# Kernel optimization log

Hardware: AMD Instinct MI355X
Metric: run time of the kernel (lower is better)

Reference implementation:

```python
import jax, jax.numpy as jnp
import numpy as np
import math

B, T, DIM = 2, 2048, 4096
N_HEADS, N_KV_HEADS = 32, 8
HEAD_DIM = DIM // N_HEADS          # 128
N_REP = N_HEADS // N_KV_HEADS      # 4
ROPE_THETA = 500000.0
NEG_INF = -1e9


def setup_inputs() -> dict:
    key = jax.random.key(0)
    ks = jax.random.split(key, 5)
    x = jax.random.normal(ks[0], (B, T, DIM), dtype=jnp.float32)
    # rotary angles: theta_j = pos * base^(-2j/d), shape [T, HEAD_DIM//2]
    inv_freq = 1.0 / (ROPE_THETA ** (jnp.arange(0, HEAD_DIM, 2, dtype=jnp.float32) / HEAD_DIM))
    freqs = jnp.arange(T, dtype=jnp.float32)[:, None] * inv_freq[None, :]
    # causal additive mask [T, T]
    mask = jnp.where(jnp.tril(jnp.ones((T, T), dtype=bool)), 0.0, NEG_INF).astype(jnp.float32)
    s = 0.02
    wq = jax.random.normal(ks[1], (DIM, N_HEADS * HEAD_DIM), dtype=jnp.float32) * s
    wk = jax.random.normal(ks[2], (DIM, N_KV_HEADS * HEAD_DIM), dtype=jnp.float32) * s
    wv = jax.random.normal(ks[3], (DIM, N_KV_HEADS * HEAD_DIM), dtype=jnp.float32) * s
    wo = jax.random.normal(ks[4], (N_HEADS * HEAD_DIM, DIM), dtype=jnp.float32) * s
    return {"x": x, "freqs": freqs, "mask": mask, "wq": wq, "wk": wk, "wv": wv, "wo": wo, "start_pos": 0}


def _apply_rope(x, cos, sin):
    # x: [B, T, H, D]; cos/sin: [T, D//2]; adjacent pairs rotated (view-as-complex)
    xr = x[..., 0::2]
    xi = x[..., 1::2]
    c = cos[None, :, None, :]
    s = sin[None, :, None, :]
    out_r = xr * c - xi * s
    out_i = xr * s + xi * c
    return jnp.stack([out_r, out_i], axis=-1).reshape(x.shape)


def reference(x, freqs, mask, wq, wk, wv, wo, start_pos):
    Bx, Tx, C = x.shape
    xq = (x @ wq).reshape(Bx, Tx, N_HEADS, HEAD_DIM)
    xk = (x @ wk).reshape(Bx, Tx, N_KV_HEADS, HEAD_DIM)
    xv = (x @ wv).reshape(Bx, Tx, N_KV_HEADS, HEAD_DIM)
    cos, sin = jnp.cos(freqs), jnp.sin(freqs)
    xq = _apply_rope(xq, cos, sin)
    xk = _apply_rope(xk, cos, sin)
    # repeat_kv for GQA: [B, T, Hkv, D] -> [B, T, Hkv*n_rep, D]
    xk = jnp.repeat(xk, N_REP, axis=2)
    xv = jnp.repeat(xv, N_REP, axis=2)
    q = xq.transpose(0, 2, 1, 3)  # [B, H, T, D]
    k = xk.transpose(0, 2, 1, 3)
    v = xv.transpose(0, 2, 1, 3)
    scores = jnp.einsum("bhtd,bhsd->bhts", q, k) / math.sqrt(HEAD_DIM)
    scores = scores + mask[None, None, :, :]
    probs = jax.nn.softmax(scores.astype(jnp.float32), axis=-1).astype(q.dtype)
    out = jnp.einsum("bhts,bhsd->bhtd", probs, v)
    out = out.transpose(0, 2, 1, 3).reshape(Bx, Tx, -1)
    return out @ wo
```

## Files before the change

kernel.cpp:

```cpp
#include <hip/hip_runtime.h>
#include <cstdint>
#include <cstddef>

typedef float  f32x4  __attribute__((ext_vector_type(4)));
typedef short  bf16x8 __attribute__((ext_vector_type(8)));
typedef unsigned short u16;
typedef u16    u16x8  __attribute__((ext_vector_type(8)));

#define T_SEQ 2048
#define N_HEADS 32
#define N_KVH 8
#define HD 128

__device__ __forceinline__ u16 f2bf(float f){
  union { float f; unsigned u; } v; v.f = f;
  unsigned u = v.u;
  u += 0x7fffu + ((u >> 16) & 1u);
  return (u16)(u >> 16);
}

__device__ __forceinline__ void gll16(const void* g, void* l){
  __builtin_amdgcn_global_load_lds((const __attribute__((address_space(1))) void*)g,
                                   (__attribute__((address_space(3))) void*)l, 16, 0, 0);
}

__global__ void mk_tables(const float* __restrict__ f, float* __restrict__ c, float* __restrict__ s){
  int i = blockIdx.x*256 + threadIdx.x;
  float v = f[i];
  c[i] = cosf(v);
  s[i] = sinf(v);
}

__global__ void cvt_bf16(const float* __restrict__ in, u16* __restrict__ out){
  size_t i = (size_t)blockIdx.x*256 + threadIdx.x;
  const float4* p = (const float4*)(in + i*8);
  float4 a = p[0], b = p[1];
  u16x8 o;
  o[0]=f2bf(a.x); o[1]=f2bf(a.y); o[2]=f2bf(a.z); o[3]=f2bf(a.w);
  o[4]=f2bf(b.x); o[5]=f2bf(b.y); o[6]=f2bf(b.z); o[7]=f2bf(b.w);
  *(u16x8*)(out + i*8) = o;
}

__global__ void wtrans(const float* __restrict__ W, u16* __restrict__ Wt, int K, int N){
  __shared__ float t[32][33];
  int tx = threadIdx.x, ty = threadIdx.y;
  int nb = blockIdx.x*32, kb = blockIdx.y*32;
#pragma unroll
  for (int j=0;j<4;j++) t[ty+8*j][tx] = W[(size_t)(kb+ty+8*j)*N + nb + tx];
  __syncthreads();
#pragma unroll
  for (int j=0;j<4;j++) Wt[(size_t)(nb+ty+8*j)*K + kb + tx] = f2bf(t[tx][ty+8*j]);
}

__global__ __launch_bounds__(256) void gemm_bf16(
    const u16* __restrict__ A, const u16* __restrict__ Bt,
    float* __restrict__ C, int N, int K)
{
  __shared__ u16 Al[4096];
  __shared__ u16 Bl[4096];
  const int tid = threadIdx.x;
  const int wid = tid >> 6, lane = tid & 63;
  const int lo = lane & 15, hi = lane >> 4;
  const int m0 = blockIdx.y << 7, n0 = blockIdx.x << 7;
  const int wm = (wid >> 1)*64, wn = (wid & 1)*64;

  f32x4 acc[4][4];
#pragma unroll
  for (int i=0;i<4;i++)
#pragma unroll
    for (int j=0;j<4;j++) acc[i][j] = (f32x4){0.f,0.f,0.f,0.f};

  const int r0 = wid*32 + (lane >> 2);
  const int cb = (lane & 3)*8;
  const u16* Ag0 = A  + (size_t)(m0 + r0)*K + cb;
  const u16* Ag1 = Ag0 + (size_t)16*K;
  const u16* Bg0 = Bt + (size_t)(n0 + r0)*K + cb;
  const u16* Bg1 = Bg0 + (size_t)16*K;
  u16* Al0 = &Al[wid*1024]; u16* Al1 = Al0 + 512;
  u16* Bl0 = &Bl[wid*1024]; u16* Bl1 = Bl0 + 512;

  for (int kt = 0; kt < K; kt += 32){
    __syncthreads();
    gll16(Ag0 + kt, Al0);
    gll16(Ag1 + kt, Al1);
    gll16(Bg0 + kt, Bl0);
    gll16(Bg1 + kt, Bl1);
    __syncthreads();
    bf16x8 a[4], b[4];
#pragma unroll
    for (int i=0;i<4;i++){
      a[i] = *(const bf16x8*)&Al[(wm + i*16 + lo)*32 + hi*8];
      b[i] = *(const bf16x8*)&Bl[(wn + i*16 + lo)*32 + hi*8];
    }
#pragma unroll
    for (int i=0;i<4;i++)
#pragma unroll
      for (int j=0;j<4;j++)
        acc[i][j] = __builtin_amdgcn_mfma_f32_16x16x32_bf16(a[i], b[j], acc[i][j], 0, 0, 0);
  }

  float* Cb = C + (size_t)(m0 + wm + hi*4)*N + n0 + wn + lo;
#pragma unroll
  for (int i=0;i<4;i++)
#pragma unroll
    for (int j=0;j<4;j++)
#pragma unroll
      for (int r=0;r<4;r++)
        Cb[(size_t)(i*16 + r)*N + j*16] = acc[i][j][r];
}

__global__ __launch_bounds__(512, 2) void gemm256(
    const u16* __restrict__ A, const u16* __restrict__ Bt,
    float* __restrict__ C, int N, int K)
{
  __shared__ u16 Ab[2][16384];
  __shared__ u16 Bb[2][16384];
  const int tid = threadIdx.x;
  const int w = tid >> 6, lane = tid & 63;
  const int lo = lane & 15, hi = lane >> 4;

  const int nbx = N >> 8;
  const int cpx = (int)gridDim.x >> 3;
  const int swzb = ((int)blockIdx.x & 7)*cpx + ((int)blockIdx.x >> 3);
  const int bx = swzb % nbx, by = swzb / nbx;
  const int m0 = by << 8, n0 = bx << 8;
  const int wm = w >> 2, wn = w & 3;

  const int rA = tid >> 3;
  const int chg = (tid & 7) ^ (rA & 7);
  const size_t srcoff = (size_t)rA * K + chg*8;
  const u16* Ag = A  + (size_t)m0*K + srcoff;
  const u16* Bg = Bt + (size_t)n0*K + srcoff;
  const int dstc = (w*64)*8;

  f32x4 acc[8][4];
#pragma unroll
  for (int i=0;i<8;i++)
#pragma unroll
    for (int j=0;j<4;j++) acc[i][j] = (f32x4){0.f,0.f,0.f,0.f};

  const int NT = K >> 6;
#pragma unroll
  for (int j=0;j<4;j++) gll16(Ag + (size_t)j*64*K, &Ab[0][j*4096 + dstc]);
#pragma unroll
  for (int j=0;j<4;j++) gll16(Bg + (size_t)j*64*K, &Bb[0][j*4096 + dstc]);

  const int sw = lo & 7;
#pragma unroll 1
  for (int t=0; t<NT; ++t){
    const int cur = t & 1;
    if (t > 0){
      asm volatile("s_waitcnt lgkmcnt(0)" ::: "memory");
      __builtin_amdgcn_s_barrier();
    }
    if (t + 1 < NT){
      const int kt = (t+1) << 6;
      const int nxt = cur ^ 1;
#pragma unroll
      for (int j=0;j<4;j++) gll16(Ag + (size_t)j*64*K + kt, &Ab[nxt][j*4096 + dstc]);
#pragma unroll
      for (int j=0;j<4;j++) gll16(Bg + (size_t)j*64*K + kt, &Bb[nxt][j*4096 + dstc]);
      asm volatile("s_waitcnt vmcnt(8)" ::: "memory");
    } else {
      asm volatile("s_waitcnt vmcnt(0)" ::: "memory");
    }
    __builtin_amdgcn_s_barrier();
    __builtin_amdgcn_sched_barrier(0);

    const u16* Ac = &Ab[cur][0] + (wm*128)*64;
    const u16* Bc = &Bb[cur][0] + (wn*64)*64;
    bf16x8 a[4], b[4];
#pragma unroll
    for (int ks=0; ks<2; ks++){
      const int ch = ((ks*4 + hi) ^ sw) << 3;
#pragma unroll
      for (int g=0; g<4; g++) b[g] = *(const bf16x8*)(Bc + (g*16 + lo)*64 + ch);
#pragma unroll
      for (int mh=0; mh<2; mh++){
#pragma unroll
        for (int f=0; f<4; f++) a[f] = *(const bf16x8*)(Ac + (mh*64 + f*16 + lo)*64 + ch);
        __builtin_amdgcn_s_setprio(1);
#pragma unroll
        for (int f=0; f<4; f++)
#pragma unroll
          for (int g=0; g<4; g++)
            acc[mh*4+f][g] = __builtin_amdgcn_mfma_f32_16x16x32_bf16(a[f], b[g], acc[mh*4+f][g], 0, 0, 0);
        __builtin_amdgcn_s_setprio(0);
      }
    }
  }

#pragma unroll
  for (int mh=0; mh<2; mh++)
#pragma unroll
    for (int f=0; f<4; f++)
#pragma unroll
      for (int g=0; g<4; g++)
#pragma unroll
        for (int r=0; r<4; r++)
          C[(size_t)(m0 + wm*128 + mh*64 + f*16 + hi*4 + r)*N + n0 + wn*64 + g*16 + lo] = acc[mh*4+f][g][r];
}

__global__ void rope_q(const float* __restrict__ qf, const float* __restrict__ c,
                       const float* __restrict__ s, u16* __restrict__ qb){
  const int row = blockIdx.x;
  const int t = row & (T_SEQ-1);
  const float* ib = qf + (size_t)row*4096;
  u16* ob = qb + (size_t)row*4096;
#pragma unroll
  for (int k=0;k<8;k++){
    int p = threadIdx.x + k*256;
    int i = p & 63;
    float cv = c[t*64+i], sv = s[t*64+i];
    float2 v = *(const float2*)(ib + 2*p);
    float vr = v.x*cv - v.y*sv;
    float vi = v.x*sv + v.y*cv;
    ushort2 o; o.x = f2bf(vr*0.12751743648963412f); o.y = f2bf(vi*0.12751743648963412f);
    *(ushort2*)(ob + 2*p) = o;
  }
}

__global__ void rope_k(const float* __restrict__ kvf, const float* __restrict__ c,
                       const float* __restrict__ s, u16* __restrict__ kb){
  const int row = blockIdx.x;
  const int b = row >> 11, t = row & (T_SEQ-1);
  const float* ib = kvf + (size_t)row*2048;
#pragma unroll
  for (int k=0;k<2;k++){
    int p = threadIdx.x + k*256;
    int kvh = p >> 6, i = p & 63;
    float cv = c[t*64+i], sv = s[t*64+i];
    float2 v = *(const float2*)(ib + 2*p);
    float vr = v.x*cv - v.y*sv;
    float vi = v.x*sv + v.y*cv;
    u16* o = kb + ((size_t)(b*N_KVH+kvh)*T_SEQ + t)*HD + 2*i;
    ushort2 ov; ov.x = f2bf(vr); ov.y = f2bf(vi);
    *(ushort2*)o = ov;
  }
}

__global__ void vtrans(const float* __restrict__ kvf, u16* __restrict__ vt){
  __shared__ float tl[32][33];
  int tx = threadIdx.x, ty = threadIdx.y;
  int t0 = blockIdx.x*32, d0 = blockIdx.y*32, bh = blockIdx.z;
  int b = bh >> 3, kvh = bh & 7;
#pragma unroll
  for (int j=0;j<4;j++)
    tl[ty+8*j][tx] = kvf[(size_t)(b*T_SEQ + t0+ty+8*j)*2048 + 1024 + kvh*HD + d0 + tx];
  __syncthreads();
#pragma unroll
  for (int j=0;j<4;j++)
    vt[((size_t)bh*HD + d0+ty+8*j)*T_SEQ + t0 + tx] = f2bf(tl[tx][ty+8*j]);
}

#define KVB 64
__global__ __launch_bounds__(512, 2) void attn_kernel(
    const u16* __restrict__ qb, const u16* __restrict__ kb,
    const u16* __restrict__ vt, u16* __restrict__ attn)
{
  __shared__ u16 KV[2][2][8192];
  __shared__ u16 Pl[8][2048];

  const int tid = threadIdx.x;
  const int lane = tid & 63, wid = tid >> 6;
  const int lo = lane & 15, hi = lane >> 4;
  const int pairI = blockIdx.x;
  const int h = blockIdx.y, b = blockIdx.z;
  const int kvh = h >> 2;

  int koff[2], voff[2];
#pragma unroll
  for (int p=0;p<2;p++){
    int s = p*512 + tid;
    int kr = s >> 4, kch = (s & 15) ^ (kr & 7);
    koff[p] = kr*HD + kch*8;
    int vd = s >> 3, vch = (s & 7) ^ (vd & 7);
    voff[p] = vd*T_SEQ + vch*8;
  }
  const u16* Kg = kb + (size_t)(b*N_KVH + kvh)*T_SEQ*HD;
  const u16* Vg = vt + (size_t)(b*N_KVH + kvh)*HD*T_SEQ;

#pragma unroll 1
  for (int pass=0; pass<2; ++pass){
    const int qt = pass ? pairI : (7 - pairI);
    const int q0 = qt*256 + wid*32;
    const int ntiles = (qt+1)*4;

    bf16x8 qfr[2][4];
#pragma unroll
    for (int mb=0;mb<2;mb++){
      const u16* qrow = qb + (size_t)(b*T_SEQ + q0 + mb*16 + lo)*4096 + h*HD;
#pragma unroll
      for (int kc=0;kc<4;kc++) qfr[mb][kc] = *(const bf16x8*)(qrow + kc*32 + hi*8);
    }

    f32x4 acc[2][8];
#pragma unroll
    for (int mb=0;mb<2;mb++)
#pragma unroll
      for (int nd=0;nd<8;nd++) acc[mb][nd] = (f32x4){0.f,0.f,0.f,0.f};
    float m_[2][4], l_[2][4];
#pragma unroll
    for (int mb=0;mb<2;mb++)
#pragma unroll
      for (int r=0;r<4;r++){ m_[mb][r] = -3.0e38f; l_[mb][r] = 0.f; }

    if (pass){
      asm volatile("s_waitcnt lgkmcnt(0)" ::: "memory");
      __builtin_amdgcn_s_barrier();
    }
#pragma unroll
    for (int p=0;p<2;p++){
      gll16(Kg + koff[p], (u16*)&KV[0][0][0] + (p*512 + wid*64)*8);
      gll16(Vg + voff[p], (u16*)&KV[0][1][0] + (p*512 + wid*64)*8);
    }

#pragma unroll 1
    for (int st=0; st<ntiles; ++st){
      const int cur = st & 1;
      const int sb = st*KVB;
      if (st > 0){
        asm volatile("s_waitcnt lgkmcnt(0)" ::: "memory");
        __builtin_amdgcn_s_barrier();
      }
      if (st + 1 < ntiles){
        const int nxt = cur ^ 1;
        const int nb2 = (st+1)*KVB;
#pragma unroll
        for (int p=0;p<2;p++){
          gll16(Kg + nb2*HD + koff[p], (u16*)&KV[nxt][0][0] + (p*512 + wid*64)*8);
          gll16(Vg + nb2    + voff[p], (u16*)&KV[nxt][1][0] + (p*512 + wid*64)*8);
        }
        asm volatile("s_waitcnt vmcnt(4)" ::: "memory");
      } else {
        asm volatile("s_waitcnt vmcnt(0)" ::: "memory");
      }
      __builtin_amdgcn_s_barrier();

      const bool live = (sb <= q0 + 31);
      if (live){
        f32x4 sc[2][4];
#pragma unroll
        for (int mb=0;mb<2;mb++)
#pragma unroll
          for (int ns=0;ns<4;ns++) sc[mb][ns] = (f32x4){0.f,0.f,0.f,0.f};
        __builtin_amdgcn_s_setprio(1);
#pragma unroll
        for (int ns=0;ns<4;ns++){
          const int row = ns*16 + lo;
          const u16* klp = (const u16*)&KV[cur][0][0] + row*HD;
          const int sw = row & 7;
          bf16x8 kf[4];
#pragma unroll
          for (int kc=0;kc<4;kc++) kf[kc] = *(const bf16x8*)(klp + (((kc*4+hi)^sw)<<3));
#pragma unroll
          for (int kc=0;kc<4;kc++){
            sc[0][ns] = __builtin_amdgcn_mfma_f32_16x16x32_bf16(qfr[0][kc], kf[kc], sc[0][ns], 0, 0, 0);
            sc[1][ns] = __builtin_amdgcn_mfma_f32_16x16x32_bf16(qfr[1][kc], kf[kc], sc[1][ns], 0, 0, 0);
          }
        }
        __builtin_amdgcn_s_setprio(0);

        if (sb + 63 > q0){
#pragma unroll
          for (int mb=0;mb<2;mb++)
#pragma unroll
            for (int ns=0;ns<4;ns++)
#pragma unroll
              for (int r=0;r<4;r++){
                int qg = q0 + mb*16 + hi*4 + r;
                int sg = sb + ns*16 + lo;
                if (sg > qg) sc[mb][ns][r] = -3.0e38f;
              }
        }

#pragma unroll
        for (int mb=0;mb<2;mb++){
          float mx[4], rs[4];
#pragma unroll
          for (int r=0;r<4;r++)
            mx[r] = fmaxf(fmaxf(sc[mb][0][r], sc[mb][1][r]), fmaxf(sc[mb][2][r], sc[mb][3][r]));
#pragma unroll
          for (int d=1; d<16; d<<=1)
#pragma unroll
            for (int r=0;r<4;r++) mx[r] = fmaxf(mx[r], __shfl_xor(mx[r], d));
          bool grow = false;
#pragma unroll
          for (int r=0;r<4;r++) grow |= (mx[r] > m_[mb][r] + 8.f);
          if (__any(grow)){
            float scal[4];
#pragma unroll
            for (int r=0;r<4;r++){
              float mn = fmaxf(m_[mb][r], mx[r]);
              scal[r] = exp2f(m_[mb][r] - mn);
              m_[mb][r] = mn;
            }
#pragma unroll
            for (int nd=0;nd<8;nd++)
#pragma unroll
              for (int r=0;r<4;r++) acc[mb][nd][r] *= scal[r];
#pragma unroll
            for (int r=0;r<4;r++) l_[mb][r] *= scal[r];
          }
#pragma unroll
          for (int r=0;r<4;r++){
            rs[r] = 0.f;
#pragma unroll
            for (int ns=0;ns<4;ns++){
              sc[mb][ns][r] = exp2f(sc[mb][ns][r] - m_[mb][r]);
              rs[r] += sc[mb][ns][r];
            }
          }
#pragma unroll
          for (int d=1; d<16; d<<=1)
#pragma unroll
            for (int r=0;r<4;r++) rs[r] += __shfl_xor(rs[r], d);
#pragma unroll
          for (int r=0;r<4;r++) l_[mb][r] += rs[r];
        }

        u16* pbuf = (u16*)Pl[wid];
#pragma unroll
        for (int mb=0;mb<2;mb++)
#pragma unroll
          for (int ns=0;ns<4;ns++)
#pragma unroll
            for (int r=0;r<4;r++){
              int row = mb*16 + hi*4 + r, col = ns*16 + lo;
              pbuf[row*64 + (((col>>3)^(row&7))<<3) + (col&7)] = f2bf(sc[mb][ns][r]);
            }
        asm volatile("s_waitcnt lgkmcnt(0)" ::: "memory");
        __builtin_amdgcn_sched_barrier(0);
        bf16x8 pa[2][2];
#pragma unroll
        for (int mb=0;mb<2;mb++){
          const int row = mb*16 + lo;
#pragma unroll
          for (int k2=0;k2<2;k2++)
            pa[mb][k2] = *(const bf16x8*)(pbuf + row*64 + (((k2*4+hi)^(row&7))<<3));
        }

        __builtin_amdgcn_s_setprio(1);
#pragma unroll
        for (int nd=0;nd<8;nd++){
          const int d = nd*16 + lo;
          const u16* vlp = (const u16*)&KV[cur][1][0] + d*64;
          const int sw = d & 7;
          bf16x8 vf[2];
#pragma unroll
          for (int k2=0;k2<2;k2++) vf[k2] = *(const bf16x8*)(vlp + (((k2*4+hi)^sw)<<3));
#pragma unroll
          for (int k2=0;k2<2;k2++){
            acc[0][nd] = __builtin_amdgcn_mfma_f32_16x16x32_bf16(pa[0][k2], vf[k2], acc[0][nd], 0, 0, 0);
            acc[1][nd] = __builtin_amdgcn_mfma_f32_16x16x32_bf16(pa[1][k2], vf[k2], acc[1][nd], 0, 0, 0);
          }
        }
        __builtin_amdgcn_s_setprio(0);
      }
    }

    float inv[2][4];
#pragma unroll
    for (int mb=0;mb<2;mb++)
#pragma unroll
      for (int r=0;r<4;r++) inv[mb][r] = 1.f / l_[mb][r];
#pragma unroll
    for (int mb=0;mb<2;mb++){
      u16* ob = attn + (size_t)(b*T_SEQ + q0 + mb*16 + hi*4)*4096 + h*HD;
#pragma unroll
      for (int nd=0;nd<8;nd++)
#pragma unroll
        for (int r=0;r<4;r++)
          ob[(size_t)r*4096 + nd*16 + lo] = f2bf(acc[mb][nd][r]*inv[mb][r]);
    }
  }
}

extern "C" void kernel_launch(void* const* d_in, const int* in_sizes, int n_in,
                              void* d_out, int out_size, void* d_ws, size_t ws_size,
                              hipStream_t stream)
{
  (void)in_sizes; (void)n_in; (void)out_size; (void)ws_size;
  const float* x     = (const float*)d_in[0];
  const float* freqs = (const float*)d_in[1];
  const float* wq    = (const float*)d_in[3];
  const float* wk    = (const float*)d_in[4];
  const float* wv    = (const float*)d_in[5];
  const float* wo    = (const float*)d_in[6];

  char* ws = (char*)d_ws;
  float* cost = (float*)(ws + 0);
  float* sint = (float*)(ws + 524288);
  u16* xb   = (u16*)(ws + 1048576);
  u16* wqt  = (u16*)(ws + 34603008);
  u16* wkt  = (u16*)(ws + 68157440);
  u16* wvt  = (u16*)(ws + 76546048);
  u16* qbuf = (u16*)(ws + 84934656);
  u16* kbuf = (u16*)(ws + 118489088);
  u16* vbuf = (u16*)(ws + 126877696);
  u16* attnb = xb;
  u16* wot   = wqt;

  float* qf  = (float*)d_out;
  float* kvf = (float*)d_out;

  dim3 tb(32, 8);

  mk_tables<<<512, 256, 0, stream>>>(freqs, cost, sint);
  cvt_bf16<<<8192, 256, 0, stream>>>(x, xb);
  wtrans<<<dim3(128,128), tb, 0, stream>>>(wq, wqt, 4096, 4096);
  wtrans<<<dim3(32,128),  tb, 0, stream>>>(wk, wkt, 4096, 1024);
  wtrans<<<dim3(32,128),  tb, 0, stream>>>(wv, wvt, 4096, 1024);

  gemm256<<<dim3(256), 512, 0, stream>>>(xb, wqt, qf, 4096, 4096);
  rope_q<<<4096, 256, 0, stream>>>(qf, cost, sint, qbuf);

  gemm_bf16<<<dim3(16,32), 256, 0, stream>>>(xb, wkt, kvf, 2048, 4096);
  rope_k<<<4096, 256, 0, stream>>>(kvf, cost, sint, kbuf);
  vtrans<<<dim3(64,4,16), tb, 0, stream>>>(kvf, vbuf);

  attn_kernel<<<dim3(4,32,2), 512, 0, stream>>>(qbuf, kbuf, vbuf, attnb);

  wtrans<<<dim3(128,128), tb, 0, stream>>>(wo, wot, 4096, 4096);
  gemm256<<<dim3(256), 512, 0, stream>>>(attnb, wot, (float*)d_out, 4096, 4096);
}
```

Baseline: 617.1 us.

## Compute transposed scores, keep P in registers via lane shuffles, reuse gemm256 for KV

The score MFMA now computes K·Q^T, so each lane holds one query row. That makes row max and row sum mostly in-lane reductions with only two cross-lane shuffles. The probability tile is packed to bf16 with v_cvt_pk_bf16_f32 and rearranged into the PV operand layout through register shuffles, which removes the per-wave LDS P buffer and its wait. The launch bound is relaxed from (512,2) to (512), and the small KV projection GEMM is replaced by the larger 256-tile gemm256 kernel. The trade-offs are more shuffle instructions, possibly higher register pressure, and fewer blocks for the KV GEMM.

```diff
diff --git a/kernel.cpp b/kernel.cpp
--- a/kernel.cpp
+++ b/kernel.cpp
@@ -6,6 +6,7 @@
 typedef short  bf16x8 __attribute__((ext_vector_type(8)));
 typedef unsigned short u16;
 typedef u16    u16x8  __attribute__((ext_vector_type(8)));
+typedef unsigned int u32;
 
 #define T_SEQ 2048
 #define N_HEADS 32
@@ -17,6 +18,12 @@
   unsigned u = v.u;
   u += 0x7fffu + ((u >> 16) & 1u);
   return (u16)(u >> 16);
+}
+
+__device__ __forceinline__ u32 cvt_pk_bf16(float a, float b){
+  u32 r;
+  asm volatile("v_cvt_pk_bf16_f32 %0, %1, %2" : "=v"(r) : "v"(a), "v"(b));
+  return r;
 }
 
 __device__ __forceinline__ void gll16(const void* g, void* l){
@@ -50,63 +57,6 @@
   __syncthreads();
 #pragma unroll
   for (int j=0;j<4;j++) Wt[(size_t)(nb+ty+8*j)*K + kb + tx] = f2bf(t[tx][ty+8*j]);
-}
-
-__global__ __launch_bounds__(256) void gemm_bf16(
-    const u16* __restrict__ A, const u16* __restrict__ Bt,
-    float* __restrict__ C, int N, int K)
-{
-  __shared__ u16 Al[4096];
-  __shared__ u16 Bl[4096];
-  const int tid = threadIdx.x;
-  const int wid = tid >> 6, lane = tid & 63;
-  const int lo = lane & 15, hi = lane >> 4;
-  const int m0 = blockIdx.y << 7, n0 = blockIdx.x << 7;
-  const int wm = (wid >> 1)*64, wn = (wid & 1)*64;
-
-  f32x4 acc[4][4];
-#pragma unroll
-  for (int i=0;i<4;i++)
-#pragma unroll
-    for (int j=0;j<4;j++) acc[i][j] = (f32x4){0.f,0.f,0.f,0.f};
-
-  const int r0 = wid*32 + (lane >> 2);
-  const int cb = (lane & 3)*8;
-  const u16* Ag0 = A  + (size_t)(m0 + r0)*K + cb;
-  const u16* Ag1 = Ag0 + (size_t)16*K;
-  const u16* Bg0 = Bt + (size_t)(n0 + r0)*K + cb;
-  const u16* Bg1 = Bg0 + (size_t)16*K;
-  u16* Al0 = &Al[wid*1024]; u16* Al1 = Al0 + 512;
-  u16* Bl0 = &Bl[wid*1024]; u16* Bl1 = Bl0 + 512;
-
-  for (int kt = 0; kt < K; kt += 32){
-    __syncthreads();
-    gll16(Ag0 + kt, Al0);
-    gll16(Ag1 + kt, Al1);
-    gll16(Bg0 + kt, Bl0);
-    gll16(Bg1 + kt, Bl1);
-    __syncthreads();
-    bf16x8 a[4], b[4];
-#pragma unroll
-    for (int i=0;i<4;i++){
-      a[i] = *(const bf16x8*)&Al[(wm + i*16 + lo)*32 + hi*8];
-      b[i] = *(const bf16x8*)&Bl[(wn + i*16 + lo)*32 + hi*8];
-    }
-#pragma unroll
-    for (int i=0;i<4;i++)
-#pragma unroll
-      for (int j=0;j<4;j++)
-        acc[i][j] = __builtin_amdgcn_mfma_f32_16x16x32_bf16(a[i], b[j], acc[i][j], 0, 0, 0);
-  }
-
-  float* Cb = C + (size_t)(m0 + wm + hi*4)*N + n0 + wn + lo;
-#pragma unroll
-  for (int i=0;i<4;i++)
-#pragma unroll
-    for (int j=0;j<4;j++)
-#pragma unroll
-      for (int r=0;r<4;r++)
-        Cb[(size_t)(i*16 + r)*N + j*16] = acc[i][j][r];
 }
 
 __global__ __launch_bounds__(512, 2) void gemm256(
@@ -254,16 +204,18 @@
 }
 
 #define KVB 64
-__global__ __launch_bounds__(512, 2) void attn_kernel(
+__global__ __launch_bounds__(512) void attn_kernel(
     const u16* __restrict__ qb, const u16* __restrict__ kb,
     const u16* __restrict__ vt, u16* __restrict__ attn)
 {
   __shared__ u16 KV[2][2][8192];
-  __shared__ u16 Pl[8][2048];
 
   const int tid = threadIdx.x;
   const int lane = tid & 63, wid = tid >> 6;
   const int lo = lane & 15, hi = lane >> 4;
+  const bool lowhi = (hi < 2);
+  const int bp0 = lo + 32*(hi & 1);
+  const int bp1 = bp0 + 16;
   const int pairI = blockIdx.x;
   const int h = blockIdx.y, b = blockIdx.z;
   const int kvh = h >> 2;
@@ -299,11 +251,8 @@
     for (int mb=0;mb<2;mb++)
 #pragma unroll
       for (int nd=0;nd<8;nd++) acc[mb][nd] = (f32x4){0.f,0.f,0.f,0.f};
-    float m_[2][4], l_[2][4];
-#pragma unroll
-    for (int mb=0;mb<2;mb++)
-#pragma unroll
-      for (int r=0;r<4;r++){ m_[mb][r] = -3.0e38f; l_[mb][r] = 0.f; }
+    float m_[2] = {-3.0e38f, -3.0e38f};
+    float l_[2] = {0.f, 0.f};
 
     if (pass){
       asm volatile("s_waitcnt lgkmcnt(0)" ::: "memory");
@@ -355,89 +304,82 @@
           for (int kc=0;kc<4;kc++) kf[kc] = *(const bf16x8*)(klp + (((kc*4+hi)^sw)<<3));
 #pragma unroll
           for (int kc=0;kc<4;kc++){
-            sc[0][ns] = __builtin_amdgcn_mfma_f32_16x16x32_bf16(qfr[0][kc], kf[kc], sc[0][ns], 0, 0, 0);
-            sc[1][ns] = __builtin_amdgcn_mfma_f32_16x16x32_bf16(qfr[1][kc], kf[kc], sc[1][ns], 0, 0, 0);
+            sc[0][ns] = __builtin_amdgcn_mfma_f32_16x16x32_bf16(kf[kc], qfr[0][kc], sc[0][ns], 0, 0, 0);
+            sc[1][ns] = __builtin_amdgcn_mfma_f32_16x16x32_bf16(kf[kc], qfr[1][kc], sc[1][ns], 0, 0, 0);
           }
         }
         __builtin_amdgcn_s_setprio(0);
 
         if (sb + 63 > q0){
 #pragma unroll
-          for (int mb=0;mb<2;mb++)
+          for (int mb=0;mb<2;mb++){
+            const int qg = q0 + mb*16 + lo;
 #pragma unroll
             for (int ns=0;ns<4;ns++)
 #pragma unroll
               for (int r=0;r<4;r++){
-                int qg = q0 + mb*16 + hi*4 + r;
-                int sg = sb + ns*16 + lo;
+                int sg = sb + ns*16 + hi*4 + r;
                 if (sg > qg) sc[mb][ns][r] = -3.0e38f;
               }
+          }
         }
 
+        bf16x8 pa[2][2];
 #pragma unroll
         for (int mb=0;mb<2;mb++){
-          float mx[4], rs[4];
-#pragma unroll
-          for (int r=0;r<4;r++)
-            mx[r] = fmaxf(fmaxf(sc[mb][0][r], sc[mb][1][r]), fmaxf(sc[mb][2][r], sc[mb][3][r]));
-#pragma unroll
-          for (int d=1; d<16; d<<=1)
-#pragma unroll
-            for (int r=0;r<4;r++) mx[r] = fmaxf(mx[r], __shfl_xor(mx[r], d));
-          bool grow = false;
-#pragma unroll
-          for (int r=0;r<4;r++) grow |= (mx[r] > m_[mb][r] + 8.f);
-          if (__any(grow)){
-            float scal[4];
+          float mx = fmaxf(fmaxf(fmaxf(sc[mb][0][0],sc[mb][0][1]),fmaxf(sc[mb][0][2],sc[mb][0][3])),
+                     fmaxf(fmaxf(fmaxf(sc[mb][1][0],sc[mb][1][1]),fmaxf(sc[mb][1][2],sc[mb][1][3])),
+                           fmaxf(fmaxf(sc[mb][2][0],sc[mb][2][1]),
+                                 fmaxf(fmaxf(sc[mb][2][2],sc[mb][2][3]),
+                                       fmaxf(fmaxf(sc[mb][3][0],sc[mb][3][1]),fmaxf(sc[mb][3][2],sc[mb][3][3]))))));
+          mx = fmaxf(mx, __shfl_xor(mx, 16));
+          mx = fmaxf(mx, __shfl_xor(mx, 32));
+          if (__any(mx > m_[mb] + 8.f)){
+            float mn = fmaxf(m_[mb], mx);
+            float scal = exp2f(m_[mb] - mn);
+            m_[mb] = mn;
+            l_[mb] *= scal;
+            float srow[4];
+#pragma unroll
+            for (int r=0;r<4;r++) srow[r] = __shfl(scal, hi*4+r);
+#pragma unroll
+            for (int nd=0;nd<8;nd++)
+#pragma unroll
+              for (int r=0;r<4;r++) acc[mb][nd][r] *= srow[r];
+          }
+          float rs = 0.f;
+#pragma unroll
+          for (int ns=0;ns<4;ns++)
 #pragma unroll
             for (int r=0;r<4;r++){
-              float mn = fmaxf(m_[mb][r], mx[r]);
-              scal[r] = exp2f(m_[mb][r] - mn);
-              m_[mb][r] = mn;
+              sc[mb][ns][r] = exp2f(sc[mb][ns][r] - m_[mb]);
+              rs += sc[mb][ns][r];
             }
-#pragma unroll
-            for (int nd=0;nd<8;nd++)
-#pragma unroll
-              for (int r=0;r<4;r++) acc[mb][nd][r] *= scal[r];
-#pragma unroll
-            for (int r=0;r<4;r++) l_[mb][r] *= scal[r];
+          rs += __shfl_xor(rs, 16);
+          rs += __shfl_xor(rs, 32);
+          l_[mb] += rs;
+
+#pragma unroll
+          for (int k2=0;k2<2;k2++){
+            u32 P0 = cvt_pk_bf16(sc[mb][2*k2][0],   sc[mb][2*k2][1]);
+            u32 P1 = cvt_pk_bf16(sc[mb][2*k2][2],   sc[mb][2*k2][3]);
+            u32 Q0 = cvt_pk_bf16(sc[mb][2*k2+1][0], sc[mb][2*k2+1][1]);
+            u32 Q1 = cvt_pk_bf16(sc[mb][2*k2+1][2], sc[mb][2*k2+1][3]);
+            u32 pA0 = (u32)__shfl((int)P0, bp0);
+            u32 pA1 = (u32)__shfl((int)P1, bp0);
+            u32 pA2 = (u32)__shfl((int)P0, bp1);
+            u32 pA3 = (u32)__shfl((int)P1, bp1);
+            u32 qA0 = (u32)__shfl((int)Q0, bp0);
+            u32 qA1 = (u32)__shfl((int)Q1, bp0);
+            u32 qA2 = (u32)__shfl((int)Q0, bp1);
+            u32 qA3 = (u32)__shfl((int)Q1, bp1);
+            union { u32 w[4]; bf16x8 v; } pk;
+            pk.w[0] = lowhi ? pA0 : qA0;
+            pk.w[1] = lowhi ? pA1 : qA1;
+            pk.w[2] = lowhi ? pA2 : qA2;
+            pk.w[3] = lowhi ? pA3 : qA3;
+            pa[mb][k2] = pk.v;
           }
-#pragma unroll
-          for (int r=0;r<4;r++){
-            rs[r] = 0.f;
-#pragma unroll
-            for (int ns=0;ns<4;ns++){
-              sc[mb][ns][r] = exp2f(sc[mb][ns][r] - m_[mb][r]);
-              rs[r] += sc[mb][ns][r];
-            }
-          }
-#pragma unroll
-          for (int d=1; d<16; d<<=1)
-#pragma unroll
-            for (int r=0;r<4;r++) rs[r] += __shfl_xor(rs[r], d);
-#pragma unroll
-          for (int r=0;r<4;r++) l_[mb][r] += rs[r];
-        }
-
-        u16* pbuf = (u16*)Pl[wid];
-#pragma unroll
-        for (int mb=0;mb<2;mb++)
-#pragma unroll
-          for (int ns=0;ns<4;ns++)
-#pragma unroll
-            for (int r=0;r<4;r++){
-              int row = mb*16 + hi*4 + r, col = ns*16 + lo;
-              pbuf[row*64 + (((col>>3)^(row&7))<<3) + (col&7)] = f2bf(sc[mb][ns][r]);
-            }
-        asm volatile("s_waitcnt lgkmcnt(0)" ::: "memory");
-        __builtin_amdgcn_sched_barrier(0);
-        bf16x8 pa[2][2];
-#pragma unroll
-        for (int mb=0;mb<2;mb++){
-          const int row = mb*16 + lo;
-#pragma unroll
-          for (int k2=0;k2<2;k2++)
-            pa[mb][k2] = *(const bf16x8*)(pbuf + row*64 + (((k2*4+hi)^(row&7))<<3));
         }
 
         __builtin_amdgcn_s_setprio(1);
@@ -459,19 +401,18 @@
       }
     }
 
-    float inv[2][4];
-#pragma unroll
-    for (int mb=0;mb<2;mb++)
-#pragma unroll
-      for (int r=0;r<4;r++) inv[mb][r] = 1.f / l_[mb][r];
 #pragma unroll
     for (int mb=0;mb<2;mb++){
+      float inv = 1.f / l_[mb];
+      float invr[4];
+#pragma unroll
+      for (int r=0;r<4;r++) invr[r] = __shfl(inv, hi*4+r);
       u16* ob = attn + (size_t)(b*T_SEQ + q0 + mb*16 + hi*4)*4096 + h*HD;
 #pragma unroll
       for (int nd=0;nd<8;nd++)
 #pragma unroll
         for (int r=0;r<4;r++)
-          ob[(size_t)r*4096 + nd*16 + lo] = f2bf(acc[mb][nd][r]*inv[mb][r]);
+          ob[(size_t)r*4096 + nd*16 + lo] = f2bf(acc[mb][nd][r]*invr[r]);
     }
   }
 }
@@ -515,7 +456,7 @@
   gemm256<<<dim3(256), 512, 0, stream>>>(xb, wqt, qf, 4096, 4096);
   rope_q<<<4096, 256, 0, stream>>>(qf, cost, sint, qbuf);
 
-  gemm_bf16<<<dim3(16,32), 256, 0, stream>>>(xb, wkt, kvf, 2048, 4096);
+  gemm256<<<dim3(128), 512, 0, stream>>>(xb, wkt, kvf, 2048, 4096);
   rope_k<<<4096, 256, 0, stream>>>(kvf, cost, sint, kbuf);
   vtrans<<<dim3(64,4,16), tb, 0, stream>>>(kvf, vbuf);
 
```

After: 610.7 us. About the same (-1.0%).
